# Kernel tuning notes

Measured on AMD Instinct MI355X. Metric: run time of the kernel, lower is better.

## Reference

```python
import jax, jax.numpy as jnp
import numpy as np

B, C_IN, C_OUT, H, W = 8, 256, 256, 48, 48


def setup_inputs() -> dict:
    key = jax.random.key(0)
    ks = jax.random.split(key, 8)
    s = 1.0 / np.sqrt(C_IN)
    return {
        "x1": jax.random.normal(ks[0], (B, C_IN, H, W), dtype=jnp.float32),
        "x2": jax.random.normal(ks[1], (B, C_IN, H, W), dtype=jnp.float32),
        "Wq": jax.random.normal(ks[2], (C_OUT, C_IN), dtype=jnp.float32) * s,
        "bq": jax.random.normal(ks[3], (C_OUT,), dtype=jnp.float32) * s,
        "Wk": jax.random.normal(ks[4], (C_OUT, C_IN), dtype=jnp.float32) * s,
        "bk": jax.random.normal(ks[5], (C_OUT,), dtype=jnp.float32) * s,
        "Wv": jax.random.normal(ks[6], (C_OUT, C_IN), dtype=jnp.float32) * s,
        "bv": jax.random.normal(ks[7], (C_OUT,), dtype=jnp.float32) * s,
    }


def _conv1x1(x, Wt, b):
    # x: [B,Cin,H,W], Wt: [Cout,Cin] -> [B,Cout,H,W]
    return jnp.einsum("bchw,oc->bohw", x, Wt) + b[None, :, None, None]


def reference(x1, x2, Wq, bq, Wk, bk, Wv, bv):
    q = _conv1x1(x1, Wq, bq)  # [B,C,H,W]
    k = _conv1x1(x2, Wk, bk)
    v = _conv1x1(x2, Wv, bv)
    b, c, h, w = q.shape
    n = h * w
    qf = q.reshape(b, c, n).transpose(0, 2, 1)  # [B,N,C]
    kf = k.reshape(b, c, n)                      # [B,C,N]
    vf = v.reshape(b, c, n).transpose(0, 2, 1)   # [B,N,C]
    # NOTE: faithful to source -- no 1/sqrt(d) scaling, no head split
    attn = jax.nn.softmax(jnp.einsum("bic,bcj->bij", qf, kf), axis=-1)  # [B,N,N]
    out = jnp.einsum("bij,bjc->bic", attn, vf)   # [B,N,C]
    return out.transpose(0, 2, 1).reshape(b, c, h, w)
```

## Files before the change

### kernel.cpp

```cpp
#include <hip/hip_runtime.h>
#include <cfloat>
#include <cstddef>
#include <cstdint>

#define BATCH 8
#define CDIM  256
#define NTOK  2304

typedef float    f32x4 __attribute__((ext_vector_type(4)));
typedef _Float16 f16x8 __attribute__((ext_vector_type(8)));
typedef _Float16 f16x4 __attribute__((ext_vector_type(4)));

#define MFMA16(a, b, c) __builtin_amdgcn_mfma_f32_16x16x32_f16(a, b, c, 0, 0, 0)

__device__ __forceinline__ void gl_lds16(const void* g, void* l) {
    __builtin_amdgcn_global_load_lds(
        (const __attribute__((address_space(1))) void*)g,
        (__attribute__((address_space(3))) void*)l, 16, 0, 0);
}

__global__ __launch_bounds__(256) void cast_w(
    const float* __restrict__ Wq, const float* __restrict__ Wk,
    const float* __restrict__ Wv, _Float16* __restrict__ Wh)
{
    int i = (blockIdx.x * 256 + threadIdx.x) * 4;
    const float* src = (i < 65536) ? (Wq + i)
                     : (i < 131072) ? (Wk + (i - 65536)) : (Wv + (i - 131072));
    float4 v = *(const float4*)src;
    f16x4 h = { (_Float16)v.x, (_Float16)v.y, (_Float16)v.z, (_Float16)v.w };
    *(f16x4*)(Wh + i) = h;
}

__global__ __launch_bounds__(256) void cast_x(
    const float* __restrict__ x1, const float* __restrict__ x2,
    _Float16* __restrict__ Xt1, _Float16* __restrict__ Xt2)
{
    const int tid = threadIdx.x;
    const int n0 = blockIdx.x * 64;
    const int c0 = blockIdx.y * 64;
    const int bz = blockIdx.z;
    const float* X   = (bz < 8) ? x1 : x2;
    _Float16*   Xt   = (bz < 8) ? Xt1 : Xt2;
    const int b = bz & 7;

    __shared__ _Float16 T[64][72];

    {
        const int cl = tid >> 2, nch = (tid & 3) * 16;
        const float* src = X + (size_t)(b * CDIM + c0 + cl) * NTOK + n0 + nch;
#pragma unroll
        for (int u = 0; u < 4; ++u) {
            float4 v = *(const float4*)(src + u * 4);
            T[cl][nch + u * 4 + 0] = (_Float16)v.x;
            T[cl][nch + u * 4 + 1] = (_Float16)v.y;
            T[cl][nch + u * 4 + 2] = (_Float16)v.z;
            T[cl][nch + u * 4 + 3] = (_Float16)v.w;
        }
    }
    __syncthreads();
    {
        const int nl = tid >> 2, cch = (tid & 3) * 16;
        _Float16* dst = Xt + (size_t)(b * NTOK + n0 + nl) * CDIM + c0 + cch;
        f16x8 o0, o1;
#pragma unroll
        for (int i = 0; i < 8; ++i) {
            o0[i] = T[cch + i][nl];
            o1[i] = T[cch + 8 + i][nl];
        }
        *(f16x8*)dst = o0;
        *(f16x8*)(dst + 8) = o1;
    }
}

__global__ __launch_bounds__(256, 2) void proj_mfma(
    const _Float16* __restrict__ Xt1, const _Float16* __restrict__ Xt2,
    const _Float16* __restrict__ Wh,
    const float* __restrict__ bq, const float* __restrict__ bk,
    const float* __restrict__ bv,
    _Float16* __restrict__ Qo, _Float16* __restrict__ Ko, _Float16* __restrict__ Vo)
{
    const int tid  = threadIdx.x;
    const int lane = tid & 63;
    const int w    = tid >> 6;
    const int l15  = lane & 15, l4 = lane >> 4;
    const int n0   = blockIdx.x * 64;
    const int mode = blockIdx.y;
    const int b    = blockIdx.z;

    const _Float16* Xt = (mode == 0) ? Xt1 : Xt2;
    const _Float16* Wm = Wh + mode * 65536;
    const float* bias  = (mode == 0) ? bq : (mode == 1) ? bk : bv;
    _Float16* OUT      = (mode == 0) ? Qo : (mode == 1) ? Ko : Vo;

    __shared__ __align__(16) char sm[65536];
    _Float16* Xl = (_Float16*)sm;
    _Float16* Wl = (_Float16*)(sm + 32768);

#pragma unroll
    for (int t = 0; t < 8; ++t) {
        int i = w * 8 + t;
        int row = 2 * i + (lane >> 5);
        int ch  = lane & 31;
        gl_lds16(Xt + (size_t)(b * NTOK + n0 + row) * CDIM + ((ch ^ (row & 7)) * 8),
                 (char*)Xl + i * 1024);
    }

    float bias_o[4];
#pragma unroll
    for (int ot = 0; ot < 4; ++ot) bias_o[ot] = bias[w * 64 + ot * 16 + l15];

    f32x4 acc[16];
#pragma unroll
    for (int i = 0; i < 16; ++i) acc[i] = (f32x4){0.f, 0.f, 0.f, 0.f};

    for (int c0 = 0; c0 < CDIM; c0 += 64) {
        __syncthreads();
#pragma unroll
        for (int t = 0; t < 8; ++t) {
            int i = w * 8 + t;
            int row = 8 * i + (lane >> 3);
            int ch  = lane & 7;
            gl_lds16(Wm + (size_t)row * CDIM + c0 + ((ch ^ (row & 7)) * 8),
                     (char*)Wl + i * 1024);
        }
        __syncthreads();

#pragma unroll
        for (int kk2 = 0; kk2 < 2; ++kk2) {
            f16x8 a[4], bf[4];
#pragma unroll
            for (int nt = 0; nt < 4; ++nt) {
                int row = nt * 16 + l15;
                int ch  = ((c0 >> 3) + kk2 * 4 + l4) ^ (row & 7);
                a[nt] = *(const f16x8*)((const char*)Xl + row * 512 + ch * 16);
            }
#pragma unroll
            for (int ot = 0; ot < 4; ++ot) {
                int row = w * 64 + ot * 16 + l15;
                int ch  = (kk2 * 4 + l4) ^ (row & 7);
                bf[ot] = *(const f16x8*)((const char*)Wl + row * 128 + ch * 16);
            }
#pragma unroll
            for (int nt = 0; nt < 4; ++nt)
#pragma unroll
                for (int ot = 0; ot < 4; ++ot)
                    acc[nt * 4 + ot] = MFMA16(a[nt], bf[ot], acc[nt * 4 + ot]);
        }
    }

    __syncthreads();

    if (mode <= 1) {
        _Float16* Dl = (_Float16*)sm;
#pragma unroll
        for (int nt = 0; nt < 4; ++nt)
#pragma unroll
            for (int ot = 0; ot < 4; ++ot)
#pragma unroll
                for (int reg = 0; reg < 4; ++reg)
                    Dl[(nt * 16 + 4 * l4 + reg) * 256 + w * 64 + ot * 16 + l15] =
                        (_Float16)(acc[nt * 4 + ot][reg] + bias_o[ot]);
        __syncthreads();
        char* dst = (char*)(OUT + ((size_t)b * NTOK + n0) * CDIM);
#pragma unroll
        for (int u = 0; u < 8; ++u) {
            f16x8 v = *(const f16x8*)((const char*)Dl + u * 4096 + tid * 16);
            *(f16x8*)(dst + u * 4096 + tid * 16) = v;
        }
    } else {
        _Float16* Dlv = (_Float16*)sm;
#pragma unroll
        for (int nt = 0; nt < 4; ++nt)
#pragma unroll
            for (int ot = 0; ot < 4; ++ot)
#pragma unroll
                for (int reg = 0; reg < 4; ++reg)
                    Dlv[(w * 64 + ot * 16 + l15) * 80 + nt * 16 + 4 * l4 + reg] =
                        (_Float16)(acc[nt * 4 + ot][reg] + bias_o[ot]);
        __syncthreads();
#pragma unroll
        for (int t = 0; t < 8; ++t) {
            int ro = (w * 8 + t) * 8 + (lane >> 3);
            f16x8 v = *(const f16x8*)((const char*)Dlv + ro * 160 + (lane & 7) * 16);
            *(f16x8*)(OUT + ((size_t)b * CDIM + ro) * NTOK + n0 + (lane & 7) * 8) = v;
        }
    }
}

template <int SEG>
__global__ __launch_bounds__(512, 2) void attn_fa(
    const _Float16* __restrict__ Q, const _Float16* __restrict__ K,
    const _Float16* __restrict__ Vt, _Float16* __restrict__ pacc,
    float2* __restrict__ pml)
{
    const int tid  = threadIdx.x;
    const int lane = tid & 63;
    const int w    = tid >> 6;
    const int l15  = lane & 15, l4 = lane >> 4;

    const int nb  = 18 * BATCH * SEG, cpx = nb / 8;
    const int bid = blockIdx.x;
    const int swz = (bid & 7) * cpx + (bid >> 3);
    const int x = swz % 18;
    const int b = (swz / 18) & 7;
    const int z = swz / 144;

    const int row0   = x * 128 + w * 16;
    const int jbase  = z * (NTOK / SEG);
    const int NTILES = NTOK / SEG / 64;

    __shared__ __align__(16) char smem[147456];
    _Float16* Pw = (_Float16*)(smem + 131072 + w * 2048);

    const size_t kbb = (size_t)b * NTOK;
    const size_t vbb = (size_t)b * CDIM * NTOK;

    auto stage = [&](int j0, int buf) {
        char* Klc = smem + buf * 65536;
        char* Vlc = Klc + 32768;
#pragma unroll
        for (int t = 0; t < 4; ++t) {
            int i = w * 4 + t;
            int krow = 2 * i + (lane >> 5);
            int chunk = lane & 31;
            gl_lds16(K + (kbb + j0 + krow) * CDIM + ((chunk ^ (krow & 7)) * 8),
                     Klc + i * 1024);
        }
#pragma unroll
        for (int t = 0; t < 4; ++t) {
            int i = w * 4 + t;
            int vrow = 8 * i + (lane >> 3);
            int chunk = lane & 7;
            gl_lds16(Vt + vbb + (size_t)vrow * NTOK + j0 + ((chunk ^ (vrow & 7)) * 8),
                     Vlc + i * 1024);
        }
    };

    f16x8 qa[8];
    {
        const _Float16* qb = Q + ((size_t)b * NTOK + row0 + l15) * CDIM + l4 * 8;
#pragma unroll
        for (int kk = 0; kk < 8; ++kk)
            qa[kk] = __builtin_nontemporal_load((const f16x8*)(qb + kk * 32));
    }

    f32x4 acc[16];
#pragma unroll
    for (int ct = 0; ct < 16; ++ct) acc[ct] = (f32x4){0.f, 0.f, 0.f, 0.f};
    f32x4 accl = (f32x4){0.f, 0.f, 0.f, 0.f};
    float m[4] = {-FLT_MAX, -FLT_MAX, -FLT_MAX, -FLT_MAX};

    const f16x8 vone = {(_Float16)1.f, (_Float16)1.f, (_Float16)1.f, (_Float16)1.f,
                        (_Float16)1.f, (_Float16)1.f, (_Float16)1.f, (_Float16)1.f};

    stage(jbase, 0);
    __syncthreads();

    for (int jt = 0; jt < NTILES; ++jt) {
        const int cur = jt & 1;

        if (jt + 1 < NTILES) stage(jbase + (jt + 1) * 64, cur ^ 1);

        const char* Klc = (const char*)smem + cur * 65536;
        const char* Vlc = Klc + 32768;

        f32x4 s[4];
#pragma unroll
        for (int nt = 0; nt < 4; ++nt) {
            const char* kb = Klc + (nt * 16 + l15) * 512;
            f32x4 sv = (f32x4){0.f, 0.f, 0.f, 0.f};
#pragma unroll
            for (int kk = 0; kk < 8; ++kk) {
                f16x8 kf = *(const f16x8*)(kb + (((kk * 4 + l4) ^ (l15 & 7)) * 16));
                sv = MFMA16(qa[kk], kf, sv);
            }
            s[nt] = sv;
        }

#pragma unroll
        for (int reg = 0; reg < 4; ++reg) {
            float pm = fmaxf(fmaxf(s[0][reg], s[1][reg]),
                             fmaxf(s[2][reg], s[3][reg]));
            pm = fmaxf(pm, __shfl_xor(pm, 1));
            pm = fmaxf(pm, __shfl_xor(pm, 2));
            pm = fmaxf(pm, __shfl_xor(pm, 4));
            pm = fmaxf(pm, __shfl_xor(pm, 8));
            if (pm > m[reg] + 8.f) {
                float sc = __expf(m[reg] - pm);
                m[reg] = pm;
                accl[reg] *= sc;
#pragma unroll
                for (int ct = 0; ct < 16; ++ct) acc[ct][reg] *= sc;
            }
            const int r = 4 * l4 + reg;
#pragma unroll
            for (int nt = 0; nt < 4; ++nt) {
                float p = __expf(s[nt][reg] - m[reg]);
                int j = nt * 16 + l15;
                Pw[r * 64 + ((j >> 3) ^ (r & 7)) * 8 + (j & 7)] = (_Float16)p;
            }
        }

        asm volatile("s_waitcnt lgkmcnt(0)" ::: "memory");
        __builtin_amdgcn_sched_barrier(0);

        f16x8 pa[2];
#pragma unroll
        for (int kc = 0; kc < 2; ++kc)
            pa[kc] = *(const f16x8*)((const char*)Pw + l15 * 128
                                     + (((kc * 4 + l4) ^ (l15 & 7)) * 16));
        accl = MFMA16(pa[0], vone, accl);
        accl = MFMA16(pa[1], vone, accl);
#pragma unroll
        for (int ct = 0; ct < 16; ++ct) {
            const char* vb0 = Vlc + (ct * 16 + l15) * 128;
#pragma unroll
            for (int kc = 0; kc < 2; ++kc) {
                f16x8 vb = *(const f16x8*)(vb0 + (((kc * 4 + l4) ^ (l15 & 7)) * 16));
                acc[ct] = MFMA16(pa[kc], vb, acc[ct]);
            }
        }

        __syncthreads();
    }

    _Float16* stg = (_Float16*)(smem + w * 8192);
#pragma unroll
    for (int reg = 0; reg < 4; ++reg) {
        float inv = 1.f / accl[reg];
        int r = 4 * l4 + reg;
#pragma unroll
        for (int ct = 0; ct < 16; ++ct)
            stg[r * 256 + ct * 16 + l15] = (_Float16)(acc[ct][reg] * inv);
        if (l15 == 0)
            pml[((size_t)z * BATCH + b) * NTOK + row0 + r] =
                make_float2(m[reg], accl[reg]);
    }
    asm volatile("s_waitcnt lgkmcnt(0)" ::: "memory");
    __builtin_amdgcn_sched_barrier(0);
    {
        const char* stgc = (const char*)stg;
        char* dst = (char*)(pacc + ((size_t)z * BATCH + b) * NTOK * CDIM
                            + (size_t)row0 * CDIM);
#pragma unroll
        for (int u = 0; u < 8; ++u) {
            f16x8 v = *(const f16x8*)(stgc + u * 1024 + lane * 16);
            *(f16x8*)(dst + u * 1024 + lane * 16) = v;
        }
    }
}

template <int SEG>
__global__ __launch_bounds__(256) void merge_kernel(
    const _Float16* __restrict__ pacc, const float2* __restrict__ pml,
    float* __restrict__ out)
{
    const int tid = threadIdx.x;
    const int n0 = blockIdx.x * 64;
    const int b  = blockIdx.y;

    __shared__ float wgt[SEG][64];
    __shared__ float dinv[64];
    __shared__ float T[64][68];

    if (tid < 64) {
        int n = n0 + tid;
        float ms[SEG], ls[SEG];
#pragma unroll
        for (int s = 0; s < SEG; ++s) {
            float2 v = pml[((size_t)s * BATCH + b) * NTOK + n];
            ms[s] = v.x; ls[s] = v.y;
        }
        float M = ms[0];
#pragma unroll
        for (int s = 1; s < SEG; ++s) M = fmaxf(M, ms[s]);
        float den = 0.f;
#pragma unroll
        for (int s = 0; s < SEG; ++s) {
            float g = ls[s] * __expf(ms[s] - M);
            wgt[s][tid] = g;
            den += g;
        }
        dinv[tid] = 1.f / den;
    }
    __syncthreads();

    for (int cc = 0; cc < 4; ++cc) {
        const int nl = tid >> 2, cg = (tid & 3) * 16;
        float a[16];
#pragma unroll
        for (int u = 0; u < 16; ++u) a[u] = 0.f;
#pragma unroll
        for (int s = 0; s < SEG; ++s) {
            const _Float16* p = pacc + (((size_t)s * BATCH + b) * NTOK + n0 + nl) * CDIM
                                + cc * 64 + cg;
            f16x8 v0 = ((const f16x8*)p)[0];
            f16x8 v1 = ((const f16x8*)p)[1];
            float g = wgt[s][nl];
#pragma unroll
            for (int u = 0; u < 8; ++u) {
                a[u]     += g * (float)v0[u];
                a[8 + u] += g * (float)v1[u];
            }
        }
        float di = dinv[nl];
#pragma unroll
        for (int u = 0; u < 16; ++u) T[nl][cg + u] = a[u] * di;
        __syncthreads();

        const int cl = tid >> 2, nb2 = (tid & 3) * 16;
        float* ob = out + ((size_t)b * CDIM + cc * 64 + cl) * NTOK + n0 + nb2;
#pragma unroll
        for (int u = 0; u < 4; ++u) {
            float4 v = { T[nb2 + u * 4 + 0][cl], T[nb2 + u * 4 + 1][cl],
                         T[nb2 + u * 4 + 2][cl], T[nb2 + u * 4 + 3][cl] };
            *(float4*)&ob[u * 4] = v;
        }
        __syncthreads();
    }
}

extern "C" void kernel_launch(void* const* d_in, const int* in_sizes, int n_in,
                              void* d_out, int out_size, void* d_ws, size_t ws_size,
                              hipStream_t stream)
{
    const float* x1 = (const float*)d_in[0];
    const float* x2 = (const float*)d_in[1];
    const float* Wq = (const float*)d_in[2];
    const float* bq = (const float*)d_in[3];
    const float* Wk = (const float*)d_in[4];
    const float* bk = (const float*)d_in[5];
    const float* Wv = (const float*)d_in[6];
    const float* bv = (const float*)d_in[7];
    float* out = (float*)d_out;

    const size_t plane = (size_t)BATCH * NTOK * CDIM;
    _Float16* ws16 = (_Float16*)d_ws;
    _Float16* Q   = ws16;
    _Float16* K   = ws16 + plane;
    _Float16* Vt  = ws16 + 2 * plane;
    _Float16* Xt1 = ws16 + 3 * plane;
    _Float16* Xt2 = ws16 + 4 * plane;
    _Float16* Wh  = ws16 + 5 * plane;
    const size_t fixed16 = 5 * plane + 196608;

    auto need = [&](size_t S) {
        return fixed16 * 2 + S * plane * 2 + S * (size_t)BATCH * NTOK * 8;
    };
    const int SEG = (ws_size >= need(3)) ? 3 : (ws_size >= need(2)) ? 2 : 1;

    _Float16* pacc = ws16 + fixed16;
    float2*   pml  = (float2*)((char*)d_ws + fixed16 * 2 + (size_t)SEG * plane * 2);

    cast_w<<<dim3(192), dim3(256), 0, stream>>>(Wq, Wk, Wv, Wh);
    cast_x<<<dim3(36, 4, 16), dim3(256), 0, stream>>>(x1, x2, Xt1, Xt2);
    proj_mfma<<<dim3(36, 3, BATCH), dim3(256), 0, stream>>>(
        Xt1, Xt2, Wh, bq, bk, bv, Q, K, Vt);

    const int nb = 18 * BATCH;
    if (SEG == 3) {
        attn_fa<3><<<dim3(nb * 3), dim3(512), 0, stream>>>(Q, K, Vt, pacc, pml);
        merge_kernel<3><<<dim3(36, BATCH), dim3(256), 0, stream>>>(pacc, pml, out);
    } else if (SEG == 2) {
        attn_fa<2><<<dim3(nb * 2), dim3(512), 0, stream>>>(Q, K, Vt, pacc, pml);
        merge_kernel<2><<<dim3(36, BATCH), dim3(256), 0, stream>>>(pacc, pml, out);
    } else {
        attn_fa<1><<<dim3(nb), dim3(512), 0, stream>>>(Q, K, Vt, pacc, pml);
        merge_kernel<1><<<dim3(36, BATCH), dim3(256), 0, stream>>>(pacc, pml, out);
    }
}
```

Before: 133.7 us.

## Keep softmax probabilities in registers by transposing MFMA operand roles

The QK^T and PV MFMAs now take their operands swapped, and K rows are permuted when staged. As a result the score accumulator layout matches the A-operand layout the PV MFMA needs. P can then be exponentiated straight into registers, removing the per-tile LDS write/read round trip, its wait, and the dedicated P shared buffer. Each lane now owns a single query row, so the row max needs only two cross-lane shuffles. The output staging uses a padded stride to avoid bank conflicts. The trade-off is a more intricate index permutation, which must exactly match the MFMA register layout for correctness.

```diff
diff --git a/kernel.cpp b/kernel.cpp
--- a/kernel.cpp
+++ b/kernel.cpp
@@ -209,8 +209,7 @@
     const int jbase  = z * (NTOK / SEG);
     const int NTILES = NTOK / SEG / 64;
 
-    __shared__ __align__(16) char smem[147456];
-    _Float16* Pw = (_Float16*)(smem + 131072 + w * 2048);
+    __shared__ __align__(16) char smem[131072];
 
     const size_t kbb = (size_t)b * NTOK;
     const size_t vbb = (size_t)b * CDIM * NTOK;
@@ -220,10 +219,11 @@
         char* Vlc = Klc + 32768;
 #pragma unroll
         for (int t = 0; t < 4; ++t) {
-            int i = w * 4 + t;
-            int krow = 2 * i + (lane >> 5);
+            int i  = w * 4 + t;
+            int lr = 2 * i + (lane >> 5);
+            int gr = (lr & 32) | ((lr & 12) << 1) | ((lr & 16) >> 2) | (lr & 3);
             int chunk = lane & 31;
-            gl_lds16(K + (kbb + j0 + krow) * CDIM + ((chunk ^ (krow & 7)) * 8),
+            gl_lds16(K + (kbb + j0 + gr) * CDIM + ((chunk ^ (lr & 7)) * 8),
                      Klc + i * 1024);
         }
 #pragma unroll
@@ -248,7 +248,7 @@
 #pragma unroll
     for (int ct = 0; ct < 16; ++ct) acc[ct] = (f32x4){0.f, 0.f, 0.f, 0.f};
     f32x4 accl = (f32x4){0.f, 0.f, 0.f, 0.f};
-    float m[4] = {-FLT_MAX, -FLT_MAX, -FLT_MAX, -FLT_MAX};
+    float m = -FLT_MAX;
 
     const f16x8 vone = {(_Float16)1.f, (_Float16)1.f, (_Float16)1.f, (_Float16)1.f,
                         (_Float16)1.f, (_Float16)1.f, (_Float16)1.f, (_Float16)1.f};
@@ -272,69 +272,62 @@
 #pragma unroll
             for (int kk = 0; kk < 8; ++kk) {
                 f16x8 kf = *(const f16x8*)(kb + (((kk * 4 + l4) ^ (l15 & 7)) * 16));
-                sv = MFMA16(qa[kk], kf, sv);
+                sv = MFMA16(kf, qa[kk], sv);
             }
             s[nt] = sv;
         }
 
-#pragma unroll
-        for (int reg = 0; reg < 4; ++reg) {
-            float pm = fmaxf(fmaxf(s[0][reg], s[1][reg]),
-                             fmaxf(s[2][reg], s[3][reg]));
-            pm = fmaxf(pm, __shfl_xor(pm, 1));
-            pm = fmaxf(pm, __shfl_xor(pm, 2));
-            pm = fmaxf(pm, __shfl_xor(pm, 4));
-            pm = fmaxf(pm, __shfl_xor(pm, 8));
-            if (pm > m[reg] + 8.f) {
-                float sc = __expf(m[reg] - pm);
-                m[reg] = pm;
-                accl[reg] *= sc;
-#pragma unroll
-                for (int ct = 0; ct < 16; ++ct) acc[ct][reg] *= sc;
-            }
-            const int r = 4 * l4 + reg;
-#pragma unroll
-            for (int nt = 0; nt < 4; ++nt) {
-                float p = __expf(s[nt][reg] - m[reg]);
-                int j = nt * 16 + l15;
-                Pw[r * 64 + ((j >> 3) ^ (r & 7)) * 8 + (j & 7)] = (_Float16)p;
-            }
-        }
-
-        asm volatile("s_waitcnt lgkmcnt(0)" ::: "memory");
-        __builtin_amdgcn_sched_barrier(0);
+        float pm = fmaxf(fmaxf(s[0][0], s[0][1]), fmaxf(s[0][2], s[0][3]));
+        pm = fmaxf(pm, fmaxf(fmaxf(s[1][0], s[1][1]), fmaxf(s[1][2], s[1][3])));
+        pm = fmaxf(pm, fmaxf(fmaxf(s[2][0], s[2][1]), fmaxf(s[2][2], s[2][3])));
+        pm = fmaxf(pm, fmaxf(fmaxf(s[3][0], s[3][1]), fmaxf(s[3][2], s[3][3])));
+        pm = fmaxf(pm, __shfl_xor(pm, 16));
+        pm = fmaxf(pm, __shfl_xor(pm, 32));
+        if (pm > m + 8.f) {
+            float sc = __expf(m - pm);
+            m = pm;
+#pragma unroll
+            for (int e = 0; e < 4; ++e) accl[e] *= sc;
+#pragma unroll
+            for (int ct = 0; ct < 16; ++ct)
+#pragma unroll
+                for (int e = 0; e < 4; ++e) acc[ct][e] *= sc;
+        }
 
         f16x8 pa[2];
 #pragma unroll
         for (int kc = 0; kc < 2; ++kc)
-            pa[kc] = *(const f16x8*)((const char*)Pw + l15 * 128
-                                     + (((kc * 4 + l4) ^ (l15 & 7)) * 16));
-        accl = MFMA16(pa[0], vone, accl);
-        accl = MFMA16(pa[1], vone, accl);
+#pragma unroll
+            for (int e = 0; e < 8; ++e)
+                pa[kc][e] = (_Float16)__expf(s[2 * kc + (e >> 2)][e & 3] - m);
+
+        accl = MFMA16(vone, pa[0], accl);
+        accl = MFMA16(vone, pa[1], accl);
 #pragma unroll
         for (int ct = 0; ct < 16; ++ct) {
             const char* vb0 = Vlc + (ct * 16 + l15) * 128;
 #pragma unroll
             for (int kc = 0; kc < 2; ++kc) {
                 f16x8 vb = *(const f16x8*)(vb0 + (((kc * 4 + l4) ^ (l15 & 7)) * 16));
-                acc[ct] = MFMA16(pa[kc], vb, acc[ct]);
+                acc[ct] = MFMA16(vb, pa[kc], acc[ct]);
             }
         }
 
         __syncthreads();
     }
 
-    _Float16* stg = (_Float16*)(smem + w * 8192);
-#pragma unroll
-    for (int reg = 0; reg < 4; ++reg) {
-        float inv = 1.f / accl[reg];
-        int r = 4 * l4 + reg;
-#pragma unroll
-        for (int ct = 0; ct < 16; ++ct)
-            stg[r * 256 + ct * 16 + l15] = (_Float16)(acc[ct][reg] * inv);
-        if (l15 == 0)
-            pml[((size_t)z * BATCH + b) * NTOK + row0 + r] =
-                make_float2(m[reg], accl[reg]);
+    _Float16* stg = (_Float16*)(smem + w * 8448);
+    {
+        float inv = 1.f / accl[0];
+#pragma unroll
+        for (int ct = 0; ct < 16; ++ct) {
+            f16x4 o = { (_Float16)(acc[ct][0] * inv), (_Float16)(acc[ct][1] * inv),
+                        (_Float16)(acc[ct][2] * inv), (_Float16)(acc[ct][3] * inv) };
+            *(f16x4*)&stg[l15 * 264 + ct * 16 + l4 * 4] = o;
+        }
+        if (l4 == 0)
+            pml[((size_t)z * BATCH + b) * NTOK + row0 + l15] =
+                make_float2(m, accl[0]);
     }
     asm volatile("s_waitcnt lgkmcnt(0)" ::: "memory");
     __builtin_amdgcn_sched_barrier(0);
@@ -344,8 +337,9 @@
                             + (size_t)row0 * CDIM);
 #pragma unroll
         for (int u = 0; u < 8; ++u) {
-            f16x8 v = *(const f16x8*)(stgc + u * 1024 + lane * 16);
-            *(f16x8*)(dst + u * 1024 + lane * 16) = v;
+            int r = 2 * u + (lane >> 5);
+            f16x8 v = *(const f16x8*)(stgc + r * 528 + (lane & 31) * 16);
+            *(f16x8*)(dst + r * 512 + (lane & 31) * 16) = v;
         }
     }
 }
```

Result: faster. 121.2 us (-9.3%).
